# Performance work log

Hardware: AMD Instinct MI355X
Metric: run time of the kernel (lower is better)

## Reference

```python
import jax, jax.numpy as jnp
import numpy as np

EPS = 1e-6  # clamp epsilon in GeM
NORM_EPS = 1e-12  # torch F.normalize eps
PATCH_SIZES = (3,)


def l2norm(x, axis):
    n = jnp.sqrt(jnp.sum(x * x, axis=axis, keepdims=True))
    return x / jnp.maximum(n, NORM_EPS)


def setup_inputs() -> dict:
    key = jax.random.key(0)
    k1, k2, k3 = jax.random.split(key, 3)
    N, D, H, W, F = 16, 2048, 32, 32, 512
    x = jax.random.normal(k1, (N, D, H, W), jnp.float32)
    proj_w = jax.random.normal(k2, (F, D), jnp.float32) * (1.0 / np.sqrt(D))
    proj_b = jax.random.normal(k3, (F,), jnp.float32) * 0.01
    p = jnp.full((1,), 3.0, jnp.float32)
    return {"x": x, "proj_w": proj_w, "proj_b": proj_b, "p": p}


def reference(x, proj_w, proj_b, p):
    # ---- GeM global descriptor (global_pool path inside local_pool) ----
    x = l2norm(x, axis=1)                                  # L2 over channel dim
    g = jnp.clip(x, EPS, None) ** p[0]                     # [N,D,H,W]
    g = g.mean(axis=(-2, -1))                              # [N,D]
    g = g ** (1.0 / p[0])
    g = g @ proj_w.T + proj_b                              # [N,F]
    g = l2norm(g, axis=1)

    # ---- integral image over spatial dims ----
    integ = jnp.cumsum(jnp.cumsum(x, axis=-1), axis=-2)    # [N,D,H,W]

    local_descs = []
    for ps in PATCH_SIZES:
        off = ps // 2
        # zero-pad (1+off) on top/left, then replicate-pad off on bottom/right
        ipad = jnp.pad(integ, ((0, 0), (0, 0), (1 + off, 0), (1 + off, 0)))
        ipad = jnp.pad(ipad, ((0, 0), (0, 0), (0, off), (0, off)), mode='edge')
        # box sum via 4-corner integral-image difference
        # == grouped 2x2 conv with dilation=ps, weights [[1,-1],[-1,1]], stride=1
        box = (ipad[:, :, :-ps, :-ps] - ipad[:, :, :-ps, ps:]
               - ipad[:, :, ps:, :-ps] + ipad[:, :, ps:, ps:])  # [N,D,H,W]
        N, D, Hh, Ww = box.shape
        pd = box.reshape(N, D, Hh * Ww).transpose(0, 2, 1)  # [N,HW,D]
        pd = pd @ proj_w.T + proj_b                         # [N,HW,F]
        pd = l2norm(pd, axis=2)
        local_descs.append(pd.transpose(0, 2, 1))           # [N,F,HW]

    return g, local_descs[0]
```

## Files before the change

kernel.cpp:

```cpp
#include <hip/hip_runtime.h>
#include <hip/hip_bf16.h>

#define N_ 16
#define D_ 2048
#define H_ 32
#define W_ 32
#define HW_ 1024
#define F_ 512

typedef unsigned short u16;
typedef unsigned int u32;
typedef __attribute__((ext_vector_type(8))) short bf16x8;
typedef __attribute__((ext_vector_type(4))) float f32x4;

__device__ __forceinline__ u16 f2bf(float f) {
  union { float fv; u32 u; } c; c.fv = f;
  u32 u = c.u;
  u32 r = (u + 0x7fffu + ((u >> 16) & 1u)) >> 16;
  return (u16)r;
}

#define GLD_LDS16(gp, lp) __builtin_amdgcn_global_load_lds( \
    (const __attribute__((address_space(1))) void*)(gp), \
    (__attribute__((address_space(3))) void*)(lp), 16, 0, 0)

__global__ __launch_bounds__(256) void k_zero(float* __restrict__ p) {
  int i = blockIdx.x * 256 + threadIdx.x;
  ((float4*)p)[i] = (float4){0.f, 0.f, 0.f, 0.f};
}

__global__ __launch_bounds__(256) void k_sumsq(const float* __restrict__ x, float* __restrict__ sumsq) {
  const int n = blockIdx.x;
  const int dc = blockIdx.y;
  const int t = threadIdx.x;
  const float* xp = x + ((size_t)n * D_ + (size_t)dc * 64) * HW_;
  float s0 = 0.f, s1 = 0.f, s2 = 0.f, s3 = 0.f;
  for (int d = 0; d < 64; ++d) {
    const float* row = xp + (size_t)d * HW_;
    float v0 = row[t], v1 = row[t + 256], v2 = row[t + 512], v3 = row[t + 768];
    s0 += v0 * v0; s1 += v1 * v1; s2 += v2 * v2; s3 += v3 * v3;
  }
  atomicAdd(&sumsq[n * HW_ + t      ], s0);
  atomicAdd(&sumsq[n * HW_ + t + 256], s1);
  atomicAdd(&sumsq[n * HW_ + t + 512], s2);
  atomicAdd(&sumsq[n * HW_ + t + 768], s3);
}

__global__ __launch_bounds__(256) void k_box2(const float* __restrict__ x,
    const float* __restrict__ sumsq, const float* __restrict__ pvec,
    float* __restrict__ gbuf, u16* __restrict__ packA) {
  const int n = blockIdx.x, ht = blockIdx.y, dc = blockIdx.z;
  const int h0 = ht * 4, d0 = dc * 64;
  const int t = threadIdx.x;
  const int w = t & 31, g = t >> 5;
  const float p = pvec[0];
  const bool p3 = (p == 3.0f);

  __shared__ __align__(16) u16 sbox[128 * 68];

  float rn[6];
  #pragma unroll
  for (int jj = 0; jj < 6; ++jj) {
    int hp = h0 - 1 + jj;
    float r = 0.f;
    if (hp >= 0 && hp < H_) r = 1.0f / fmaxf(sqrtf(sumsq[n * HW_ + hp * W_ + w]), 1e-12f);
    rn[jj] = r;
  }

  float s[8];
  #pragma unroll
  for (int j = 0; j < 8; ++j) s[j] = 0.f;

  #pragma unroll 2
  for (int j = 0; j < 8; ++j) {
    const int d = d0 + g * 8 + j;
    const float* col = x + ((size_t)(n * D_ + d)) * HW_ + w;
    float v[6];
    #pragma unroll
    for (int jj = 0; jj < 6; ++jj) {
      int hp = h0 - 1 + jj;
      float xv = (hp >= 0 && hp < H_) ? col[hp * W_] : 0.f;
      v[jj] = xv * rn[jj];
    }
    #pragma unroll
    for (int jj = 1; jj <= 4; ++jj) {
      float cv = fmaxf(v[jj], 1e-6f);
      s[j] += p3 ? cv * cv * cv : __powf(cv, p);
    }
    float hs[6];
    #pragma unroll
    for (int jj = 0; jj < 6; ++jj) {
      float l = __shfl_up(v[jj], 1, 32);
      float r = __shfl_down(v[jj], 1, 32);
      if (w == 0) l = 0.f;
      if (w == 31) r = 0.f;
      hs[jj] = l + v[jj] + r;
    }
    #pragma unroll
    for (int k = 0; k < 4; ++k) {
      float b = hs[k] + hs[k + 1] + hs[k + 2];
      sbox[(k * 32 + w) * 68 + g * 8 + j] = f2bf(b);
    }
  }
  __syncthreads();

  {
    const int r = t >> 1, half = t & 1;
    const u16* srcp = sbox + r * 68 + half * 32;
    uint2 a[8];
    #pragma unroll
    for (int q = 0; q < 8; ++q) a[q] = *(const uint2*)(srcp + q * 4);
    const int mt = n * 16 + ht * 2 + (r >> 6);
    const int mf = (r >> 4) & 3, r15 = r & 15;
    const int kt = dc * 2 + half;
    u16* dst = packA + ((size_t)(mt * 64 + kt) * 4 + mf) * 512 + r15 * 8;
    #pragma unroll
    for (int q = 0; q < 4; ++q) {
      uint4 b;
      b.x = a[2 * q].x; b.y = a[2 * q].y; b.z = a[2 * q + 1].x; b.w = a[2 * q + 1].y;
      *(uint4*)(dst + q * 128) = b;
    }
  }

  #pragma unroll
  for (int j = 0; j < 8; ++j) {
    float v = s[j];
    v += __shfl_xor(v, 16, 32);
    v += __shfl_xor(v, 8, 32);
    v += __shfl_xor(v, 4, 32);
    v += __shfl_xor(v, 2, 32);
    v += __shfl_xor(v, 1, 32);
    if (w == 0) atomicAdd(&gbuf[n * D_ + d0 + g * 8 + j], v);
  }
}

__global__ __launch_bounds__(256) void k_wconv(const float* __restrict__ w, u16* __restrict__ packB) {
  const int i = blockIdx.x * 256 + threadIdx.x;
  const int lane = i & 63, nf = (i >> 6) & 3, kt = (i >> 8) & 63, wq = i >> 14;
  const int r15 = lane & 15, hi = lane >> 4;
  const int f = wq * 64 + nf * 16 + r15;
  const int k = kt * 32 + hi * 8;
  const float* src = w + (size_t)f * D_ + k;
  float4 v0 = *(const float4*)(src);
  float4 v1 = *(const float4*)(src + 4);
  u16 r[8] = { f2bf(v0.x), f2bf(v0.y), f2bf(v0.z), f2bf(v0.w),
               f2bf(v1.x), f2bf(v1.y), f2bf(v1.z), f2bf(v1.w) };
  *(uint4*)(packB + (size_t)i * 8) = *(const uint4*)r;
}

__global__ __launch_bounds__(512) void k_gemm(const u16* __restrict__ packA,
    const u16* __restrict__ packB, const float* __restrict__ bias,
    float* __restrict__ outL) {
  const int n  = blockIdx.x >> 4;
  const int mtl = blockIdx.x & 15;
  const int mt = blockIdx.x;
  const int hw0 = mtl * 64;
  const int t = threadIdx.x;
  const int lane = t & 63, wv = t >> 6;
  const int r15 = lane & 15, hi = lane >> 4;

  __shared__ __align__(16) float smem_f[128 * 68];
  __shared__ float s_sq[8][64];
  __shared__ float s_rn[64];

  f32x4 acc[4][4];
  #pragma unroll
  for (int a = 0; a < 4; ++a)
    #pragma unroll
    for (int b = 0; b < 4; ++b) acc[a][b] = (f32x4){0.f, 0.f, 0.f, 0.f};

  const u16* asrc = packA + ((size_t)(mt * 64) * 4 + (wv & 3)) * 512 + lane * 8;
  const u16* bbase = packB + (size_t)wv * 131072 + lane * 8;

#define STAGE_A(KT) GLD_LDS16(asrc + (size_t)(KT) * 2048, \
    (char*)smem_f + ((KT) & 3) * 4096 + (wv & 3) * 1024)

  STAGE_A(0);
  STAGE_A(1);
  bf16x8 bc[4], bn[4];
  #pragma unroll
  for (int nf = 0; nf < 4; ++nf) bc[nf] = *(const bf16x8*)(bbase + nf * 512);

  for (int kt = 0; kt < 64; ++kt) {
    if (kt + 2 < 64) STAGE_A(kt + 2);
    if (kt + 1 < 64) {
      #pragma unroll
      for (int nf = 0; nf < 4; ++nf)
        bn[nf] = *(const bf16x8*)(bbase + ((kt + 1) * 4 + nf) * 512);
    }
    __builtin_amdgcn_sched_barrier(0);
    if (kt < 62) {
      asm volatile("s_waitcnt vmcnt(5)" ::: "memory");
    } else if (kt == 62) {
      asm volatile("s_waitcnt vmcnt(4)" ::: "memory");
    } else {
      asm volatile("s_waitcnt vmcnt(0)" ::: "memory");
    }
    __builtin_amdgcn_sched_barrier(0);
    __builtin_amdgcn_s_barrier();
    __builtin_amdgcn_sched_barrier(0);

    const u16* sA = (const u16*)((const char*)smem_f + (kt & 3) * 4096);
    bf16x8 af[4];
    #pragma unroll
    for (int mf = 0; mf < 4; ++mf)
      af[mf] = *(const bf16x8*)(sA + mf * 512 + lane * 8);
    #pragma unroll
    for (int mf = 0; mf < 4; ++mf)
      #pragma unroll
      for (int nf = 0; nf < 4; ++nf)
        acc[mf][nf] = __builtin_amdgcn_mfma_f32_16x16x32_bf16(af[mf], bc[nf], acc[mf][nf], 0, 0, 0);
    #pragma unroll
    for (int nf = 0; nf < 4; ++nf) bc[nf] = bn[nf];
  }
#undef STAGE_A

  float badd[4];
  #pragma unroll
  for (int nf = 0; nf < 4; ++nf) badd[nf] = bias[wv * 64 + nf * 16 + r15];
  #pragma unroll
  for (int mf = 0; mf < 4; ++mf)
    #pragma unroll
    for (int nf = 0; nf < 4; ++nf)
      #pragma unroll
      for (int j = 0; j < 4; ++j) acc[mf][nf][j] += badd[nf];

  #pragma unroll
  for (int mf = 0; mf < 4; ++mf)
    #pragma unroll
    for (int j = 0; j < 4; ++j) {
      float s = 0.f;
      #pragma unroll
      for (int nf = 0; nf < 4; ++nf) { float v = acc[mf][nf][j]; s += v * v; }
      s += __shfl_xor(s, 1); s += __shfl_xor(s, 2); s += __shfl_xor(s, 4); s += __shfl_xor(s, 8);
      if ((lane & 15) == 0) s_sq[wv][mf * 16 + hi * 4 + j] = s;
    }
  __syncthreads();
  if (t < 64) {
    float s = 0.f;
    #pragma unroll
    for (int w8 = 0; w8 < 8; ++w8) s += s_sq[w8][t];
    s_rn[t] = 1.0f / fmaxf(sqrtf(s), 1e-12f);
  }
  __syncthreads();

  float* ct = smem_f;
  for (int nf = 0; nf < 4; ++nf) {
    const int fi = wv * 16 + r15;
    #pragma unroll
    for (int mf = 0; mf < 4; ++mf)
      #pragma unroll
      for (int j = 0; j < 4; ++j) {
        int m = mf * 16 + hi * 4 + j;
        ct[fi * 68 + m] = acc[mf][nf][j] * s_rn[m];
      }
    __syncthreads();
    {
      int fr = t >> 2, mq = t & 3;
      int f = (fr >> 4) * 64 + nf * 16 + (fr & 15);
      float* dst = outL + ((size_t)(n * F_ + f)) * HW_ + hw0 + mq * 16;
      const float* srcp = ct + fr * 68 + mq * 16;
      float4 a0 = *(const float4*)(srcp);
      float4 a1 = *(const float4*)(srcp + 4);
      float4 a2 = *(const float4*)(srcp + 8);
      float4 a3 = *(const float4*)(srcp + 12);
      *(float4*)(dst) = a0; *(float4*)(dst + 4) = a1;
      *(float4*)(dst + 8) = a2; *(float4*)(dst + 12) = a3;
    }
    __syncthreads();
  }
}

__global__ __launch_bounds__(256) void k_gem_fin(const float* __restrict__ gbuf,
    const float* __restrict__ pvec, float* __restrict__ gg) {
  int i = blockIdx.x * 256 + threadIdx.x;
  float p = pvec[0];
  float m = gbuf[i] * (1.0f / 1024.0f);
  gg[i] = (p == 3.0f) ? cbrtf(m) : powf(m, 1.0f / p);
}

__global__ __launch_bounds__(256) void k_gproj(const float* __restrict__ w,
    const float* __restrict__ bias, const float* __restrict__ gg,
    float* __restrict__ gproj) {
  const int f = blockIdx.x;
  const int t = threadIdx.x;
  float wreg[8];
  #pragma unroll
  for (int j = 0; j < 8; ++j) wreg[j] = w[(size_t)f * D_ + t + j * 256];
  __shared__ float red[4];
  const int lane = t & 63, wv = t >> 6;
  for (int n = 0; n < N_; ++n) {
    float s = 0.f;
    #pragma unroll
    for (int j = 0; j < 8; ++j) s += wreg[j] * gg[n * D_ + t + j * 256];
    #pragma unroll
    for (int off = 32; off >= 1; off >>= 1) s += __shfl_down(s, off);
    if (lane == 0) red[wv] = s;
    __syncthreads();
    if (t == 0) gproj[n * F_ + f] = red[0] + red[1] + red[2] + red[3] + bias[f];
    __syncthreads();
  }
}

__global__ __launch_bounds__(512) void k_gnorm(const float* __restrict__ gproj, float* __restrict__ outg) {
  const int n = blockIdx.x;
  const int t = threadIdx.x;
  float v = gproj[n * F_ + t];
  float s = v * v;
  const int lane = t & 63, wv = t >> 6;
  #pragma unroll
  for (int off = 32; off >= 1; off >>= 1) s += __shfl_down(s, off);
  __shared__ float red[8];
  __shared__ float rtot;
  if (lane == 0) red[wv] = s;
  __syncthreads();
  if (t == 0) {
    float a = 0.f;
    #pragma unroll
    for (int i = 0; i < 8; ++i) a += red[i];
    rtot = 1.0f / fmaxf(sqrtf(a), 1e-12f);
  }
  __syncthreads();
  outg[n * F_ + t] = v * rtot;
}

extern "C" void kernel_launch(void* const* d_in, const int* in_sizes, int n_in,
                              void* d_out, int out_size, void* d_ws, size_t ws_size,
                              hipStream_t stream) {
  const float* x  = (const float*)d_in[0];
  const float* pw = (const float*)d_in[1];
  const float* pb = (const float*)d_in[2];
  const float* pv = (const float*)d_in[3];
  float* out = (float*)d_out;

  char* ws = (char*)d_ws;
  float* sumsq = (float*)ws;
  float* gbuf  = (float*)(ws + 65536);
  float* gg    = (float*)(ws + 65536 + 131072);
  float* gproj = (float*)(ws + 65536 + 2 * 131072);
  u16*   packB = (u16*)(ws + 65536 + 2 * 131072 + 32768);
  u16*   packA = (u16*)(ws + 4u * 1024u * 1024u);

  k_zero<<<dim3(48), dim3(256), 0, stream>>>(sumsq);
  k_sumsq<<<dim3(16, 32), dim3(256), 0, stream>>>(x, sumsq);
  k_wconv<<<dim3(512), dim3(256), 0, stream>>>(pw, packB);
  k_box2<<<dim3(16, 8, 32), dim3(256), 0, stream>>>(x, sumsq, pv, gbuf, packA);
  k_gem_fin<<<dim3(128), dim3(256), 0, stream>>>(gbuf, pv, gg);
  k_gproj<<<dim3(512), dim3(256), 0, stream>>>(pw, pb, gg, gproj);
  k_gnorm<<<dim3(16), dim3(512), 0, stream>>>(gproj, out);
  k_gemm<<<dim3(256), dim3(512), 0, stream>>>(packA, packB, pb, out + N_ * F_);
}
```

Baseline: 151.4 us.

## Split GEMM over F halves with atomic row norms and separate normalize pass

The local-descriptor GEMM now launches 512 blocks of 256 threads, each covering half of the F dimension, instead of 256 blocks of 512 threads covering all of F. Per-row sums of squares are accumulated with global atomics, and a new elementwise kernel rescales the whole 32 MB output by the inverse norms. This raises block count and occupancy for the GEMM. In exchange it adds a full extra read-modify-write of the output and another launch. k_zero is enlarged to also clear the rowsq buffer.

```diff
diff --git a/kernel.cpp b/kernel.cpp
--- a/kernel.cpp
+++ b/kernel.cpp
@@ -148,20 +148,20 @@
   *(uint4*)(packB + (size_t)i * 8) = *(const uint4*)r;
 }
 
-__global__ __launch_bounds__(512) void k_gemm(const u16* __restrict__ packA,
+__global__ __launch_bounds__(256) void k_gemm(const u16* __restrict__ packA,
     const u16* __restrict__ packB, const float* __restrict__ bias,
-    float* __restrict__ outL) {
-  const int n  = blockIdx.x >> 4;
-  const int mtl = blockIdx.x & 15;
-  const int mt = blockIdx.x;
-  const int hw0 = mtl * 64;
+    float* __restrict__ rowsq, float* __restrict__ outC) {
+  const int bid = blockIdx.x;
+  const int mt = bid >> 1;
+  const int c  = bid & 1;
+  const int n  = mt >> 4;
+  const int hw0 = (mt & 15) * 64;
   const int t = threadIdx.x;
   const int lane = t & 63, wv = t >> 6;
   const int r15 = lane & 15, hi = lane >> 4;
 
-  __shared__ __align__(16) float smem_f[128 * 68];
-  __shared__ float s_sq[8][64];
-  __shared__ float s_rn[64];
+  __shared__ __align__(16) float smem_f[64 * 68];
+  __shared__ float s_sq[4][64];
 
   f32x4 acc[4][4];
   #pragma unroll
@@ -169,11 +169,11 @@
     #pragma unroll
     for (int b = 0; b < 4; ++b) acc[a][b] = (f32x4){0.f, 0.f, 0.f, 0.f};
 
-  const u16* asrc = packA + ((size_t)(mt * 64) * 4 + (wv & 3)) * 512 + lane * 8;
-  const u16* bbase = packB + (size_t)wv * 131072 + lane * 8;
+  const u16* asrc = packA + ((size_t)(mt * 64) * 4 + wv) * 512 + lane * 8;
+  const u16* bbase = packB + (size_t)(c * 4 + wv) * 131072 + lane * 8;
 
 #define STAGE_A(KT) GLD_LDS16(asrc + (size_t)(KT) * 2048, \
-    (char*)smem_f + ((KT) & 3) * 4096 + (wv & 3) * 1024)
+    (char*)smem_f + ((KT) & 3) * 4096 + wv * 1024)
 
   STAGE_A(0);
   STAGE_A(1);
@@ -217,7 +217,7 @@
 
   float badd[4];
   #pragma unroll
-  for (int nf = 0; nf < 4; ++nf) badd[nf] = bias[wv * 64 + nf * 16 + r15];
+  for (int nf = 0; nf < 4; ++nf) badd[nf] = bias[(c * 4 + wv) * 64 + nf * 16 + r15];
   #pragma unroll
   for (int mf = 0; mf < 4; ++mf)
     #pragma unroll
@@ -233,16 +233,13 @@
       #pragma unroll
       for (int nf = 0; nf < 4; ++nf) { float v = acc[mf][nf][j]; s += v * v; }
       s += __shfl_xor(s, 1); s += __shfl_xor(s, 2); s += __shfl_xor(s, 4); s += __shfl_xor(s, 8);
-      if ((lane & 15) == 0) s_sq[wv][mf * 16 + hi * 4 + j] = s;
+      if (r15 == 0) s_sq[wv][mf * 16 + hi * 4 + j] = s;
     }
   __syncthreads();
   if (t < 64) {
-    float s = 0.f;
-    #pragma unroll
-    for (int w8 = 0; w8 < 8; ++w8) s += s_sq[w8][t];
-    s_rn[t] = 1.0f / fmaxf(sqrtf(s), 1e-12f);
-  }
-  __syncthreads();
+    float s = s_sq[0][t] + s_sq[1][t] + s_sq[2][t] + s_sq[3][t];
+    atomicAdd(&rowsq[mt * 64 + t], s);
+  }
 
   float* ct = smem_f;
   for (int nf = 0; nf < 4; ++nf) {
@@ -252,13 +249,13 @@
       #pragma unroll
       for (int j = 0; j < 4; ++j) {
         int m = mf * 16 + hi * 4 + j;
-        ct[fi * 68 + m] = acc[mf][nf][j] * s_rn[m];
+        ct[fi * 68 + m] = acc[mf][nf][j];
       }
     __syncthreads();
     {
       int fr = t >> 2, mq = t & 3;
-      int f = (fr >> 4) * 64 + nf * 16 + (fr & 15);
-      float* dst = outL + ((size_t)(n * F_ + f)) * HW_ + hw0 + mq * 16;
+      int f = c * 256 + (fr >> 4) * 64 + nf * 16 + (fr & 15);
+      float* dst = outC + ((size_t)(n * F_ + f)) * HW_ + hw0 + mq * 16;
       const float* srcp = ct + fr * 68 + mq * 16;
       float4 a0 = *(const float4*)(srcp);
       float4 a1 = *(const float4*)(srcp + 4);
@@ -268,6 +265,23 @@
       *(float4*)(dst + 8) = a2; *(float4*)(dst + 12) = a3;
     }
     __syncthreads();
+  }
+}
+
+__global__ __launch_bounds__(256) void k_cnorm(float* __restrict__ outC,
+    const float* __restrict__ rowsq) {
+  const int nq = (N_ * F_ * HW_) / 4;
+  for (int i = blockIdx.x * 256 + threadIdx.x; i < nq; i += 2048 * 256) {
+    const int base = i * 4;
+    const int hw = base & (HW_ - 1);
+    const int n = base >> 19;
+    float4 rq = *(const float4*)(rowsq + n * HW_ + hw);
+    float4 v = ((const float4*)outC)[i];
+    v.x *= 1.0f / fmaxf(sqrtf(rq.x), 1e-12f);
+    v.y *= 1.0f / fmaxf(sqrtf(rq.y), 1e-12f);
+    v.z *= 1.0f / fmaxf(sqrtf(rq.z), 1e-12f);
+    v.w *= 1.0f / fmaxf(sqrtf(rq.w), 1e-12f);
+    ((float4*)outC)[i] = v;
   }
 }
 
@@ -336,17 +350,19 @@
   char* ws = (char*)d_ws;
   float* sumsq = (float*)ws;
   float* gbuf  = (float*)(ws + 65536);
-  float* gg    = (float*)(ws + 65536 + 131072);
-  float* gproj = (float*)(ws + 65536 + 2 * 131072);
-  u16*   packB = (u16*)(ws + 65536 + 2 * 131072 + 32768);
+  float* rowsq = (float*)(ws + 196608);
+  float* gg    = (float*)(ws + 262144);
+  float* gproj = (float*)(ws + 393216);
+  u16*   packB = (u16*)(ws + 425984);
   u16*   packA = (u16*)(ws + 4u * 1024u * 1024u);
 
-  k_zero<<<dim3(48), dim3(256), 0, stream>>>(sumsq);
+  k_zero<<<dim3(64), dim3(256), 0, stream>>>(sumsq);
   k_sumsq<<<dim3(16, 32), dim3(256), 0, stream>>>(x, sumsq);
   k_wconv<<<dim3(512), dim3(256), 0, stream>>>(pw, packB);
   k_box2<<<dim3(16, 8, 32), dim3(256), 0, stream>>>(x, sumsq, pv, gbuf, packA);
   k_gem_fin<<<dim3(128), dim3(256), 0, stream>>>(gbuf, pv, gg);
   k_gproj<<<dim3(512), dim3(256), 0, stream>>>(pw, pb, gg, gproj);
   k_gnorm<<<dim3(16), dim3(512), 0, stream>>>(gproj, out);
-  k_gemm<<<dim3(256), dim3(512), 0, stream>>>(packA, packB, pb, out + N_ * F_);
-}
+  k_gemm<<<dim3(512), dim3(256), 0, stream>>>(packA, packB, pb, rowsq, out + N_ * F_);
+  k_cnorm<<<dim3(2048), dim3(256), 0, stream>>>(out + N_ * F_, rowsq);
+}
```

Result: slower. 162.3 us (+7.2%).

## Double GEMM M-tile to 128 rows and stage B through LDS

Applied to the files above, without the earlier changes.

The fused projection GEMM now computes 128 spatial rows per block instead of 64, halving the grid to 128 blocks so each B (weight) fragment is reused across twice as many rows. B is now staged into LDS with async global-to-LDS loads in a 3-deep ring alongside A, replacing the direct register prefetch. The box-sum kernel's packed A layout is changed to match the new 128-row tile. This cuts B traffic per output but doubles accumulator registers and uses only 128 blocks, fewer than the number of CUs, which may hurt occupancy and load balance.

```diff
diff --git a/kernel.cpp b/kernel.cpp
--- a/kernel.cpp
+++ b/kernel.cpp
@@ -110,10 +110,10 @@
     uint2 a[8];
     #pragma unroll
     for (int q = 0; q < 8; ++q) a[q] = *(const uint2*)(srcp + q * 4);
-    const int mt = n * 16 + ht * 2 + (r >> 6);
-    const int mf = (r >> 4) & 3, r15 = r & 15;
+    const int mt = n * 8 + ht;
+    const int mf = r >> 4, r15 = r & 15;
     const int kt = dc * 2 + half;
-    u16* dst = packA + ((size_t)(mt * 64 + kt) * 4 + mf) * 512 + r15 * 8;
+    u16* dst = packA + (((size_t)mt * 64 + kt) * 8 + mf) * 512 + r15 * 8;
     #pragma unroll
     for (int q = 0; q < 4; ++q) {
       uint4 b;
@@ -151,92 +151,90 @@
 __global__ __launch_bounds__(512) void k_gemm(const u16* __restrict__ packA,
     const u16* __restrict__ packB, const float* __restrict__ bias,
     float* __restrict__ outL) {
-  const int n  = blockIdx.x >> 4;
-  const int mtl = blockIdx.x & 15;
   const int mt = blockIdx.x;
-  const int hw0 = mtl * 64;
+  const int n  = mt >> 3;
+  const int hw0 = (mt & 7) * 128;
   const int t = threadIdx.x;
   const int lane = t & 63, wv = t >> 6;
   const int r15 = lane & 15, hi = lane >> 4;
 
-  __shared__ __align__(16) float smem_f[128 * 68];
-  __shared__ float s_sq[8][64];
-  __shared__ float s_rn[64];
-
-  f32x4 acc[4][4];
-  #pragma unroll
-  for (int a = 0; a < 4; ++a)
+  __shared__ __align__(16) u16 smem[3 * 20480];
+  __shared__ float s_sq[8][128];
+  __shared__ float s_rn[128];
+
+  f32x4 acc[8][4];
+  #pragma unroll
+  for (int a = 0; a < 8; ++a)
     #pragma unroll
     for (int b = 0; b < 4; ++b) acc[a][b] = (f32x4){0.f, 0.f, 0.f, 0.f};
 
-  const u16* asrc = packA + ((size_t)(mt * 64) * 4 + (wv & 3)) * 512 + lane * 8;
-  const u16* bbase = packB + (size_t)wv * 131072 + lane * 8;
-
-#define STAGE_A(KT) GLD_LDS16(asrc + (size_t)(KT) * 2048, \
-    (char*)smem_f + ((KT) & 3) * 4096 + (wv & 3) * 1024)
-
-  STAGE_A(0);
-  STAGE_A(1);
-  bf16x8 bc[4], bn[4];
-  #pragma unroll
-  for (int nf = 0; nf < 4; ++nf) bc[nf] = *(const bf16x8*)(bbase + nf * 512);
+  const u16* asrc = packA + ((size_t)mt * 64 * 8 + wv) * 512 + lane * 8;
+  const u16* bsrc = packB + (size_t)wv * 131072 + lane * 8;
+
+#define STAGE(KT) do {                                                     \
+    u16* dst_ = smem + ((KT) % 3) * 20480;                                 \
+    GLD_LDS16(asrc + (size_t)(KT) * 4096, (char*)(dst_ + wv * 512));       \
+    _Pragma("unroll")                                                      \
+    for (int q = 0; q < 4; ++q)                                            \
+      GLD_LDS16(bsrc + ((size_t)(KT) * 4 + q) * 512,                       \
+                (char*)(dst_ + 4096 + (wv * 4 + q) * 512));                \
+  } while (0)
+
+  STAGE(0);
+  STAGE(1);
 
   for (int kt = 0; kt < 64; ++kt) {
-    if (kt + 2 < 64) STAGE_A(kt + 2);
-    if (kt + 1 < 64) {
-      #pragma unroll
-      for (int nf = 0; nf < 4; ++nf)
-        bn[nf] = *(const bf16x8*)(bbase + ((kt + 1) * 4 + nf) * 512);
-    }
     __builtin_amdgcn_sched_barrier(0);
-    if (kt < 62) {
+    if (kt < 63) {
       asm volatile("s_waitcnt vmcnt(5)" ::: "memory");
-    } else if (kt == 62) {
-      asm volatile("s_waitcnt vmcnt(4)" ::: "memory");
     } else {
       asm volatile("s_waitcnt vmcnt(0)" ::: "memory");
     }
     __builtin_amdgcn_sched_barrier(0);
     __builtin_amdgcn_s_barrier();
     __builtin_amdgcn_sched_barrier(0);
-
-    const u16* sA = (const u16*)((const char*)smem_f + (kt & 3) * 4096);
-    bf16x8 af[4];
-    #pragma unroll
-    for (int mf = 0; mf < 4; ++mf)
+    if (kt <= 61) STAGE(kt + 2);
+    __builtin_amdgcn_sched_barrier(0);
+
+    const u16* sA = smem + (kt % 3) * 20480;
+    const u16* sB = sA + 4096;
+    bf16x8 af[8], bf[4];
+    #pragma unroll
+    for (int mf = 0; mf < 8; ++mf)
       af[mf] = *(const bf16x8*)(sA + mf * 512 + lane * 8);
     #pragma unroll
-    for (int mf = 0; mf < 4; ++mf)
+    for (int nf = 0; nf < 4; ++nf)
+      bf[nf] = *(const bf16x8*)(sB + (wv * 4 + nf) * 512 + lane * 8);
+    #pragma unroll
+    for (int mf = 0; mf < 8; ++mf)
       #pragma unroll
       for (int nf = 0; nf < 4; ++nf)
-        acc[mf][nf] = __builtin_amdgcn_mfma_f32_16x16x32_bf16(af[mf], bc[nf], acc[mf][nf], 0, 0, 0);
-    #pragma unroll
-    for (int nf = 0; nf < 4; ++nf) bc[nf] = bn[nf];
-  }
-#undef STAGE_A
+        acc[mf][nf] = __builtin_amdgcn_mfma_f32_16x16x32_bf16(af[mf], bf[nf], acc[mf][nf], 0, 0, 0);
+  }
+#undef STAGE
 
   float badd[4];
   #pragma unroll
   for (int nf = 0; nf < 4; ++nf) badd[nf] = bias[wv * 64 + nf * 16 + r15];
   #pragma unroll
-  for (int mf = 0; mf < 4; ++mf)
+  for (int mf = 0; mf < 8; ++mf)
     #pragma unroll
     for (int nf = 0; nf < 4; ++nf)
       #pragma unroll
       for (int j = 0; j < 4; ++j) acc[mf][nf][j] += badd[nf];
 
   #pragma unroll
-  for (int mf = 0; mf < 4; ++mf)
+  for (int mf = 0; mf < 8; ++mf)
     #pragma unroll
     for (int j = 0; j < 4; ++j) {
       float s = 0.f;
       #pragma unroll
       for (int nf = 0; nf < 4; ++nf) { float v = acc[mf][nf][j]; s += v * v; }
       s += __shfl_xor(s, 1); s += __shfl_xor(s, 2); s += __shfl_xor(s, 4); s += __shfl_xor(s, 8);
-      if ((lane & 15) == 0) s_sq[wv][mf * 16 + hi * 4 + j] = s;
-    }
-  __syncthreads();
-  if (t < 64) {
+      if (r15 == 0) s_sq[wv][mf * 16 + hi * 4 + j] = s;
+    }
+  __syncthreads();
+  if (t < 128) {
     float s = 0.f;
     #pragma unroll
     for (int w8 = 0; w8 < 8; ++w8) s += s_sq[w8][t];
@@ -244,28 +242,25 @@
   }
   __syncthreads();
 
-  float* ct = smem_f;
+  float* ct = (float*)smem;
   for (int nf = 0; nf < 4; ++nf) {
     const int fi = wv * 16 + r15;
     #pragma unroll
-    for (int mf = 0; mf < 4; ++mf)
+    for (int mf = 0; mf < 8; ++mf)
       #pragma unroll
       for (int j = 0; j < 4; ++j) {
         int m = mf * 16 + hi * 4 + j;
-        ct[fi * 68 + m] = acc[mf][nf][j] * s_rn[m];
+        ct[fi * 132 + m] = acc[mf][nf][j] * s_rn[m];
       }
     __syncthreads();
     {
       int fr = t >> 2, mq = t & 3;
       int f = (fr >> 4) * 64 + nf * 16 + (fr & 15);
-      float* dst = outL + ((size_t)(n * F_ + f)) * HW_ + hw0 + mq * 16;
-      const float* srcp = ct + fr * 68 + mq * 16;
-      float4 a0 = *(const float4*)(srcp);
-      float4 a1 = *(const float4*)(srcp + 4);
-      float4 a2 = *(const float4*)(srcp + 8);
-      float4 a3 = *(const float4*)(srcp + 12);
-      *(float4*)(dst) = a0; *(float4*)(dst + 4) = a1;
-      *(float4*)(dst + 8) = a2; *(float4*)(dst + 12) = a3;
+      float* dst = outL + ((size_t)(n * F_ + f)) * HW_ + hw0 + mq * 32;
+      const float* srcp = ct + fr * 132 + mq * 32;
+      #pragma unroll
+      for (int q = 0; q < 8; ++q)
+        ((float4*)dst)[q] = ((const float4*)srcp)[q];
     }
     __syncthreads();
   }
@@ -348,5 +343,5 @@
   k_gem_fin<<<dim3(128), dim3(256), 0, stream>>>(gbuf, pv, gg);
   k_gproj<<<dim3(512), dim3(256), 0, stream>>>(pw, pb, gg, gproj);
   k_gnorm<<<dim3(16), dim3(512), 0, stream>>>(gproj, out);
-  k_gemm<<<dim3(256), dim3(512), 0, stream>>>(packA, packB, pb, out + N_ * F_);
-}
+  k_gemm<<<dim3(128), dim3(512), 0, stream>>>(packA, packB, pb, out + N_ * F_);
+}
```

Result: slower. 195.1 us (+28.9%).

## Vectorize box-filter loads to float4 per thread with shared inverse norms

Applied to the files above, without the earlier changes.

Remaps k_box2 threads so that each handles 4 adjacent columns and 2 channels using float4 global loads instead of 1 column and 8 channels with scalar loads. The inverse L2 norms are computed once into shared memory rather than redundantly per thread. The horizontal 3-tap sum now uses in-register neighbours with only one edge shuffle, and the GeM reductions shrink to 3 shuffle steps. The cost is scattered 2-byte LDS stores into sbox with more bank conflicts, and an extra barrier.

```diff
diff --git a/kernel.cpp b/kernel.cpp
--- a/kernel.cpp
+++ b/kernel.cpp
@@ -52,54 +52,75 @@
   const int n = blockIdx.x, ht = blockIdx.y, dc = blockIdx.z;
   const int h0 = ht * 4, d0 = dc * 64;
   const int t = threadIdx.x;
-  const int w = t & 31, g = t >> 5;
+  const int w4 = t & 7, dg = t >> 3;
+  const int wq = w4 * 4;
   const float p = pvec[0];
   const bool p3 = (p == 3.0f);
 
   __shared__ __align__(16) u16 sbox[128 * 68];
-
-  float rn[6];
-  #pragma unroll
-  for (int jj = 0; jj < 6; ++jj) {
+  __shared__ __align__(16) float rnl[6][32];
+
+  if (t < 192) {
+    int jj = t >> 5, w = t & 31;
     int hp = h0 - 1 + jj;
     float r = 0.f;
     if (hp >= 0 && hp < H_) r = 1.0f / fmaxf(sqrtf(sumsq[n * HW_ + hp * W_ + w]), 1e-12f);
-    rn[jj] = r;
-  }
-
-  float s[8];
-  #pragma unroll
-  for (int j = 0; j < 8; ++j) s[j] = 0.f;
-
-  #pragma unroll 2
-  for (int j = 0; j < 8; ++j) {
-    const int d = d0 + g * 8 + j;
-    const float* col = x + ((size_t)(n * D_ + d)) * HW_ + w;
-    float v[6];
+    rnl[jj][w] = r;
+  }
+  __syncthreads();
+
+  float s0 = 0.f, s1 = 0.f;
+  #pragma unroll
+  for (int dj = 0; dj < 2; ++dj) {
+    const int d = d0 + dg * 2 + dj;
+    const float* base = x + ((size_t)(n * D_ + d)) * HW_ + wq;
+    float4 v[6];
     #pragma unroll
     for (int jj = 0; jj < 6; ++jj) {
       int hp = h0 - 1 + jj;
-      float xv = (hp >= 0 && hp < H_) ? col[hp * W_] : 0.f;
-      v[jj] = xv * rn[jj];
-    }
+      if (hp >= 0 && hp < H_) {
+        float4 xv = *(const float4*)(base + hp * W_);
+        float4 rr = *(const float4*)(&rnl[jj][wq]);
+        v[jj].x = xv.x * rr.x; v[jj].y = xv.y * rr.y;
+        v[jj].z = xv.z * rr.z; v[jj].w = xv.w * rr.w;
+      } else {
+        v[jj] = (float4){0.f, 0.f, 0.f, 0.f};
+      }
+    }
+    float g = 0.f;
     #pragma unroll
     for (int jj = 1; jj <= 4; ++jj) {
-      float cv = fmaxf(v[jj], 1e-6f);
-      s[j] += p3 ? cv * cv * cv : __powf(cv, p);
-    }
-    float hs[6];
+      float cx = fmaxf(v[jj].x, 1e-6f), cy = fmaxf(v[jj].y, 1e-6f);
+      float cz = fmaxf(v[jj].z, 1e-6f), cw = fmaxf(v[jj].w, 1e-6f);
+      if (p3) g += cx * cx * cx + cy * cy * cy + cz * cz * cz + cw * cw * cw;
+      else    g += __powf(cx, p) + __powf(cy, p) + __powf(cz, p) + __powf(cw, p);
+    }
+    if (dj == 0) s0 = g; else s1 = g;
     #pragma unroll
     for (int jj = 0; jj < 6; ++jj) {
-      float l = __shfl_up(v[jj], 1, 32);
-      float r = __shfl_down(v[jj], 1, 32);
-      if (w == 0) l = 0.f;
-      if (w == 31) r = 0.f;
-      hs[jj] = l + v[jj] + r;
+      float lf = __shfl_up(v[jj].w, 1, 8);
+      float rf = __shfl_down(v[jj].x, 1, 8);
+      if (w4 == 0) lf = 0.f;
+      if (w4 == 7) rf = 0.f;
+      float4 h;
+      h.x = lf + v[jj].x + v[jj].y;
+      h.y = v[jj].x + v[jj].y + v[jj].z;
+      h.z = v[jj].y + v[jj].z + v[jj].w;
+      h.w = v[jj].z + v[jj].w + rf;
+      v[jj] = h;
     }
     #pragma unroll
     for (int k = 0; k < 4; ++k) {
-      float b = hs[k] + hs[k + 1] + hs[k + 2];
-      sbox[(k * 32 + w) * 68 + g * 8 + j] = f2bf(b);
+      float4 b;
+      b.x = v[k].x + v[k + 1].x + v[k + 2].x;
+      b.y = v[k].y + v[k + 1].y + v[k + 2].y;
+      b.z = v[k].z + v[k + 1].z + v[k + 2].z;
+      b.w = v[k].w + v[k + 1].w + v[k + 2].w;
+      const int rb = k * 32 + wq;
+      sbox[(rb + 0) * 68 + dg * 2 + dj] = f2bf(b.x);
+      sbox[(rb + 1) * 68 + dg * 2 + dj] = f2bf(b.y);
+      sbox[(rb + 2) * 68 + dg * 2 + dj] = f2bf(b.z);
+      sbox[(rb + 3) * 68 + dg * 2 + dj] = f2bf(b.w);
     }
   }
   __syncthreads();
@@ -122,15 +143,15 @@
     }
   }
 
-  #pragma unroll
-  for (int j = 0; j < 8; ++j) {
-    float v = s[j];
-    v += __shfl_xor(v, 16, 32);
-    v += __shfl_xor(v, 8, 32);
-    v += __shfl_xor(v, 4, 32);
-    v += __shfl_xor(v, 2, 32);
-    v += __shfl_xor(v, 1, 32);
-    if (w == 0) atomicAdd(&gbuf[n * D_ + d0 + g * 8 + j], v);
+  {
+    float v0 = s0, v1 = s1;
+    v0 += __shfl_xor(v0, 1, 8); v1 += __shfl_xor(v1, 1, 8);
+    v0 += __shfl_xor(v0, 2, 8); v1 += __shfl_xor(v1, 2, 8);
+    v0 += __shfl_xor(v0, 4, 8); v1 += __shfl_xor(v1, 4, 8);
+    if (w4 == 0) {
+      atomicAdd(&gbuf[n * D_ + d0 + dg * 2    ], v0);
+      atomicAdd(&gbuf[n * D_ + d0 + dg * 2 + 1], v1);
+    }
   }
 }
 
```

After: 139.7 us (median of 2 runs). -7.7%, faster.
